# Performance work log

Measured on AMD Instinct MI355X. Metric: run time of the kernel, lower is better.

Reference implementation:

```python
import jax, jax.numpy as jnp
import numpy as np

EMBED_DIM = 1024
NUM_HEADS = 16
HEAD_DIM = EMBED_DIM // NUM_HEADS
ROPE_BASE = 10000.0


def setup_inputs() -> dict:
    key = jax.random.key(0)
    ks = jax.random.split(key, 12)
    B, T, M, D = 4, 2048, 2048, EMBED_DIM
    query = jax.random.normal(ks[0], (B, T, D), dtype=jnp.float32)
    k_in = jax.random.normal(ks[1], (B, M, D), dtype=jnp.float32)
    v_in = jax.random.normal(ks[2], (B, M, D), dtype=jnp.float32)
    query_position_ids = jnp.sort(
        jax.random.randint(ks[3], (B, T), 0, 4096), axis=-1
    ).astype(jnp.int64)
    # xavier-uniform-ish projection weights, zero biases (as in _reset_parameters)
    lim = float(np.sqrt(6.0 / (D + D)))
    Wq = jax.random.uniform(ks[4], (D, D), minval=-lim, maxval=lim, dtype=jnp.float32)
    Wk = jax.random.uniform(ks[5], (D, D), minval=-lim, maxval=lim, dtype=jnp.float32)
    Wv = jax.random.uniform(ks[6], (D, D), minval=-lim, maxval=lim, dtype=jnp.float32)
    Wo = jax.random.uniform(ks[7], (D, D), minval=-lim, maxval=lim, dtype=jnp.float32)
    bq = jnp.zeros((D,), jnp.float32)
    bk = jnp.zeros((D,), jnp.float32)
    bv = jnp.zeros((D,), jnp.float32)
    bo = jnp.zeros((D,), jnp.float32)
    return dict(query=query, key=k_in, value=v_in,
                query_position_ids=query_position_ids,
                Wq=Wq, bq=bq, Wk=Wk, bk=bk, Wv=Wv, bv=bv, Wo=Wo, bo=bo)


def _apply_rope(q, position_ids):
    # q: [B, T, H, hd]; position_ids: [B, T]
    hd = q.shape[-1]
    inv_freq = 1.0 / (ROPE_BASE ** (jnp.arange(0, hd, 2, dtype=jnp.float32) / hd))
    ang = position_ids.astype(jnp.float32)[:, :, None] * inv_freq  # [B, T, hd/2]
    cos = jnp.cos(ang)[:, :, None, :]  # [B, T, 1, hd/2]
    sin = jnp.sin(ang)[:, :, None, :]
    q1, q2 = q[..., : hd // 2], q[..., hd // 2:]
    return jnp.concatenate([q1 * cos - q2 * sin, q2 * cos + q1 * sin], axis=-1)


def reference(query, key, value, query_position_ids, Wq, bq, Wk, bk, Wv, bv, Wo, bo):
    B, T, D = query.shape
    M = key.shape[1]
    H, hd = NUM_HEADS, HEAD_DIM
    scaling = 1.0 / np.sqrt(hd)
    q = (query @ Wq.T + bq).reshape(B, T, H, hd)
    k = (key @ Wk.T + bk).reshape(B, M, H, hd)
    v = (value @ Wv.T + bv).reshape(B, M, H, hd)
    q = _apply_rope(q, query_position_ids)
    # scores: [B, H, T, M]
    scores = jnp.einsum('bthd,bmhd->bhtm', q, k) * scaling
    attn = jax.nn.softmax(scores, axis=-1)
    out = jnp.einsum('bhtm,bmhd->bthd', attn, v).reshape(B, T, D)
    return out @ Wo.T + bo
```

## Files before the change

### kernel.cpp

```cpp
#include <hip/hip_runtime.h>
#include <hip/hip_bf16.h>
#include <math.h>

typedef __hip_bfloat16 bf16;
typedef __attribute__((ext_vector_type(8))) short bf16x8;
typedef __attribute__((ext_vector_type(4))) float f32x4;

#define D_MODEL 1024
#define N_HEADS 16
#define HEAD_D  64
#define SEQ     2048
#define BATCH   4
#define NROWS   (BATCH*SEQ)

#define SCALE_Q 0.18033688011112042f

#define MFMA(a,b,c) __builtin_amdgcn_mfma_f32_16x16x32_bf16(a,b,c,0,0,0)

#if __has_builtin(__builtin_amdgcn_exp2f)
#define EXP2(x) __builtin_amdgcn_exp2f(x)
#else
#define EXP2(x) exp2f(x)
#endif

__device__ __forceinline__ void gload16(void* lds_uniform_base, const void* g) {
  __builtin_amdgcn_global_load_lds(
      (const __attribute__((address_space(1))) void*)g,
      (__attribute__((address_space(3))) void*)lds_uniform_base,
      16, 0, 0);
}

__device__ __forceinline__ unsigned pkrne(float a, float b) {
  unsigned ua = __float_as_uint(a), ub = __float_as_uint(b);
  ua += 0x7FFFu + ((ua >> 16) & 1u);
  ub += 0x7FFFu + ((ub >> 16) & 1u);
  return (ua >> 16) | (ub & 0xFFFF0000u);
}
__device__ __forceinline__ unsigned cvtpk(float a, float b) {
  unsigned r;
  asm("v_cvt_pk_bf16_f32 %0, %1, %2" : "=v"(r) : "v"(a), "v"(b));
  return r;
}
__device__ __forceinline__ bf16x8 cvt8rne(float4 a, float4 b) {
  union { bf16x8 v; unsigned u[4]; } u;
  u.u[0] = pkrne(a.x, a.y); u.u[1] = pkrne(a.z, a.w);
  u.u[2] = pkrne(b.x, b.y); u.u[3] = pkrne(b.z, b.w);
  return u.v;
}

__global__ __launch_bounds__(256)
void convw(const float* __restrict__ src, bf16* __restrict__ dst) {
  int idx = (blockIdx.x * 256 + threadIdx.x) * 8;
  float4 a = *(const float4*)(src + idx);
  float4 b = *(const float4*)(src + idx + 4);
  *(bf16x8*)(dst + idx) = cvt8rne(a, b);
}

__global__ __launch_bounds__(256)
void convw3(const float* __restrict__ s0, const float* __restrict__ s1,
            const float* __restrict__ s2, bf16* __restrict__ dst) {
  int g = blockIdx.x;
  const float* src = (g < 512) ? s0 : ((g < 1024) ? s1 : s2);
  int idx = ((g & 511) * 256 + threadIdx.x) * 8;
  float4 a = *(const float4*)(src + idx);
  float4 b = *(const float4*)(src + idx + 4);
  *(bf16x8*)(dst + (size_t)(g >> 9) * 1048576 + idx) = cvt8rne(a, b);
}

template<int MODE>
__global__ __launch_bounds__(256, 2)
void gemm_bt(const bf16* __restrict__ Xb, const bf16* __restrict__ Wb,
             const float* __restrict__ bias, void* __restrict__ outv,
             const int* __restrict__ pos) {
  __shared__ bf16 sA[128*64];
  __shared__ bf16 sB[128*64];

  const int tid  = threadIdx.x;
  const int lane = tid & 63, wid = tid >> 6;
  const int q4 = lane >> 4, l15 = lane & 15;
  const int rb = blockIdx.x * 128;
  const int cb = blockIdx.y * 128;
  const int wm = (wid >> 1) * 64, wn = (wid & 1) * 64;

  f32x4 acc[4][4];
  const f32x4 z4 = {0.f, 0.f, 0.f, 0.f};
#pragma unroll
  for (int i = 0; i < 4; ++i)
#pragma unroll
    for (int j = 0; j < 4; ++j) acc[i][j] = z4;

  for (int kt = 0; kt < 16; ++kt) {
    const int k0 = kt * 64;
#pragma unroll
    for (int i = 0; i < 4; ++i) {
      int o  = i*4096 + tid*16;
      int rr = o >> 7;
      int c0 = ((o >> 4) & 7) ^ (rr & 7);
      gload16((char*)sA + i*4096 + (wid << 10),
              Xb + (size_t)(rb + rr)*D_MODEL + k0 + c0*8);
      gload16((char*)sB + i*4096 + (wid << 10),
              Wb + (size_t)(cb + rr)*D_MODEL + k0 + c0*8);
    }
    __syncthreads();
#pragma unroll
    for (int kq = 0; kq < 2; ++kq) {
      bf16x8 af[4], bfr[4];
      const int cc = (kq*4 + q4) ^ (l15 & 7);
#pragma unroll
      for (int mi = 0; mi < 4; ++mi) {
        int r = wm + mi*16 + l15;
        af[mi] = *(const bf16x8*)((const char*)sA + r*128 + cc*16);
      }
#pragma unroll
      for (int ni = 0; ni < 4; ++ni) {
        int r = wn + ni*16 + l15;
        bfr[ni] = *(const bf16x8*)((const char*)sB + r*128 + cc*16);
      }
#pragma unroll
      for (int mi = 0; mi < 4; ++mi)
#pragma unroll
        for (int ni = 0; ni < 4; ++ni)
          acc[mi][ni] = MFMA(af[mi], bfr[ni], acc[mi][ni]);
    }
    __syncthreads();
  }

  if (MODE == 0) {
    float* outF = (float*)outv;
#pragma unroll
    for (int ni = 0; ni < 4; ++ni) {
      int col = cb + wn + ni*16 + l15;
      float bv = bias[col];
#pragma unroll
      for (int mi = 0; mi < 4; ++mi) {
        int row0 = rb + wm + mi*16 + q4*4;
#pragma unroll
        for (int r = 0; r < 4; ++r)
          outF[(size_t)(row0 + r)*D_MODEL + col] = acc[mi][ni][r] + bv;
      }
    }
  } else if (MODE == 1) {
    bf16* out = (bf16*)outv;
#pragma unroll
    for (int ni = 0; ni < 4; ++ni) {
      int col = cb + wn + ni*16 + l15;
      int h = col >> 6, d = col & 63;
      float bv = bias[col];
#pragma unroll
      for (int mi = 0; mi < 4; ++mi) {
#pragma unroll
        for (int r = 0; r < 4; ++r) {
          int row = rb + wm + mi*16 + q4*4 + r;
          int b = row >> 11, m = row & 2047;
          out[(size_t)((b*N_HEADS + h)*SEQ + m)*HEAD_D + d] =
              __float2bfloat16(acc[mi][ni][r] + bv);
        }
      }
    }
  } else if (MODE == 2) {
    bf16* out = (bf16*)outv;
#pragma unroll
    for (int mi = 0; mi < 4; ++mi) {
#pragma unroll
      for (int r = 0; r < 4; ++r) {
        int row = rb + wm + mi*16 + q4*4 + r;
        float bv = bias[row];
#pragma unroll
        for (int ni = 0; ni < 4; ++ni) {
          int col = cb + wn + ni*16 + l15;
          int b = col >> 11, m = col & 2047;
          out[(size_t)(b*D_MODEL + row)*SEQ + m] =
              __float2bfloat16(acc[mi][ni][r] + bv);
        }
      }
    }
  } else {
    bf16* out = (bf16*)outv;
    const bool is64 = (pos[NROWS - 1] == 0);
    const float CLOG = 13.287712379549449f / 32.0f;
    float invf0 = exp2f(-(float)(l15)      * CLOG);
    float invf1 = exp2f(-(float)(l15 + 16) * CLOG);
    int h = (cb + wn) >> 6;
#pragma unroll
    for (int ni = 0; ni < 2; ++ni) {
      int col1 = cb + wn + ni*16 + l15;
      int d = ni*16 + l15;
      float invf = (ni == 0) ? invf0 : invf1;
      float b1 = bias[col1];
      float b2 = bias[col1 + 32];
#pragma unroll
      for (int mi = 0; mi < 4; ++mi) {
#pragma unroll
        for (int r = 0; r < 4; ++r) {
          int row = rb + wm + mi*16 + q4*4 + r;
          int b = row >> 11, t = row & 2047;
          int pv = is64 ? pos[2*row] : pos[row];
          float ang = (float)pv * invf;
          float sn, cs;
          __sincosf(ang, &sn, &cs);
          float q1 = acc[mi][ni][r]   + b1;
          float q2 = acc[mi][ni+2][r] + b2;
          size_t base = (size_t)((b*N_HEADS + h)*SEQ + t)*HEAD_D;
          out[base + d]      = __float2bfloat16((q1*cs - q2*sn) * SCALE_Q);
          out[base + d + 32] = __float2bfloat16((q2*cs + q1*sn) * SCALE_Q);
        }
      }
    }
  }
}

__global__ __launch_bounds__(256, 2)
void attn_kernel(const bf16* __restrict__ Q, const bf16* __restrict__ K,
                 const bf16* __restrict__ VT, bf16* __restrict__ O) {
  __shared__ __align__(16) char smem[49152];
  char* sK  = smem;
  char* sVT = smem + 16384;

  const int tid  = threadIdx.x;
  const int lane = tid & 63, wid = tid >> 6;
  const int q4 = lane >> 4, l15 = lane & 15;
  const int n   = blockIdx.x;
  const int bh  = (n & 7) + 8 * (n >> 7);
  const int qb  = ((n >> 3) & 15) * 128;

  const bf16* Qp  = Q  + (size_t)bh * SEQ * HEAD_D;
  const bf16* Kp  = K  + (size_t)bh * SEQ * HEAD_D;
  const bf16* VTp = VT + (size_t)bh * HEAD_D * SEQ;
  char* wP = smem + (wid & 1) * 8192 + (wid >> 1) * 32768;

  bf16x8 qf[2][2];
#pragma unroll
  for (int mi = 0; mi < 2; ++mi)
#pragma unroll
    for (int kq = 0; kq < 2; ++kq) {
      int t = qb + wid*32 + mi*16 + l15;
      qf[mi][kq] = *(const bf16x8*)(Qp + (size_t)t*HEAD_D + kq*32 + q4*8);
    }

  const f32x4 z4 = {0.f, 0.f, 0.f, 0.f};
  f32x4 oacc[2][4];
  float mrow[2], lrow[2];
#pragma unroll
  for (int mi = 0; mi < 2; ++mi) {
#pragma unroll
    for (int nd = 0; nd < 4; ++nd) oacc[mi][nd] = z4;
    mrow[mi] = -3.0e38f; lrow[mi] = 0.f;
  }

  for (int kv = 0; kv < 16; ++kv) {
    const int m0 = kv * 128;
#pragma unroll
    for (int i = 0; i < 4; ++i) {
      int o  = i*4096 + tid*16;
      int rr = o >> 7;
      int c0 = ((o >> 4) & 7) ^ (rr & 7);
      gload16(sK + i*4096 + (wid << 10),
              Kp + (size_t)(m0 + rr)*HEAD_D + c0*8);
    }
#pragma unroll
    for (int i = 0; i < 4; ++i) {
      int o  = i*4096 + tid*16;
      int rr = o >> 8;
      int c0 = ((o >> 4) & 15) ^ (rr & 7);
      gload16(sVT + i*4096 + (wid << 10),
              VTp + (size_t)rr*SEQ + m0 + c0*8);
    }
    __syncthreads();

    f32x4 st[2][8];
#pragma unroll
    for (int mi = 0; mi < 2; ++mi)
#pragma unroll
      for (int ni = 0; ni < 8; ++ni) st[mi][ni] = z4;
#pragma unroll
    for (int kq = 0; kq < 2; ++kq) {
      const int cc = (kq*4 + q4) ^ (l15 & 7);
#pragma unroll
      for (int ni = 0; ni < 8; ++ni) {
        bf16x8 kf = *(const bf16x8*)(sK + (ni*16 + l15)*128 + cc*16);
        st[0][ni] = MFMA(kf, qf[0][kq], st[0][ni]);
        st[1][ni] = MFMA(kf, qf[1][kq], st[1][ni]);
      }
    }
    __syncthreads();

#pragma unroll
    for (int mi = 0; mi < 2; ++mi) {
      float mloc = st[mi][0][0];
#pragma unroll
      for (int ni = 0; ni < 8; ++ni)
#pragma unroll
        for (int r = 0; r < 4; ++r) mloc = fmaxf(mloc, st[mi][ni][r]);
      mloc = fmaxf(mloc, __shfl_xor(mloc, 16, 64));
      mloc = fmaxf(mloc, __shfl_xor(mloc, 32, 64));
      float mn = fmaxf(mrow[mi], mloc);
      float al = EXP2(mrow[mi] - mn);
      mrow[mi] = mn;
      float rs = 0.f;
#pragma unroll
      for (int ni = 0; ni < 8; ++ni)
#pragma unroll
        for (int r = 0; r < 4; ++r) {
          float p = EXP2(st[mi][ni][r] - mn);
          st[mi][ni][r] = p;
          rs += p;
        }
      lrow[mi] = lrow[mi]*al + rs;
#pragma unroll
      for (int nd = 0; nd < 4; ++nd)
#pragma unroll
        for (int r = 0; r < 4; ++r) oacc[mi][nd][r] *= al;
      char* rowp = wP + (mi*16 + l15)*256;
#pragma unroll
      for (int ni = 0; ni < 8; ++ni) {
        uint2 pk;
        pk.x = cvtpk(st[mi][ni][0], st[mi][ni][1]);
        pk.y = cvtpk(st[mi][ni][2], st[mi][ni][3]);
        int c  = 2*ni + (q4 >> 1);
        int cs = c ^ (l15 & 7);
        *(uint2*)(rowp + cs*16 + 8*(q4 & 1)) = pk;
      }
    }

#pragma unroll
    for (int kk = 0; kk < 4; ++kk) {
      const int cc = (kk*4 + q4) ^ (l15 & 7);
      bf16x8 vf[4];
#pragma unroll
      for (int nd = 0; nd < 4; ++nd)
        vf[nd] = *(const bf16x8*)(sVT + (nd*16 + l15)*256 + cc*16);
#pragma unroll
      for (int mi = 0; mi < 2; ++mi) {
        bf16x8 pb = *(const bf16x8*)(wP + (mi*16 + l15)*256 + cc*16);
#pragma unroll
        for (int nd = 0; nd < 4; ++nd)
          oacc[mi][nd] = MFMA(vf[nd], pb, oacc[mi][nd]);
      }
    }
    __syncthreads();
  }

  const int b = bh >> 4, h = bh & 15;
#pragma unroll
  for (int mi = 0; mi < 2; ++mi) {
    float l = lrow[mi];
    l += __shfl_xor(l, 16, 64);
    l += __shfl_xor(l, 32, 64);
    float inv = 1.0f / l;
    int t = qb + wid*32 + mi*16 + l15;
#pragma unroll
    for (int nd = 0; nd < 4; ++nd) {
      uint2 pk;
      pk.x = pkrne(oacc[mi][nd][0]*inv, oacc[mi][nd][1]*inv);
      pk.y = pkrne(oacc[mi][nd][2]*inv, oacc[mi][nd][3]*inv);
      int d = nd*16 + 4*q4;
      *(uint2*)(O + (size_t)(b*SEQ + t)*D_MODEL + h*HEAD_D + d) = pk;
    }
  }
}

extern "C" void kernel_launch(void* const* d_in, const int* in_sizes, int n_in,
                              void* d_out, int out_size, void* d_ws, size_t ws_size,
                              hipStream_t stream) {
  const float* query = (const float*)d_in[0];
  const float* key   = (const float*)d_in[1];
  const float* value = (const float*)d_in[2];
  const int*   pos   = (const int*)d_in[3];
  const float* Wq = (const float*)d_in[4];  const float* bq = (const float*)d_in[5];
  const float* Wk = (const float*)d_in[6];  const float* bk = (const float*)d_in[7];
  const float* Wv = (const float*)d_in[8];  const float* bv = (const float*)d_in[9];
  const float* Wo = (const float*)d_in[10]; const float* bo = (const float*)d_in[11];

  char* ws = (char*)d_ws;
  bf16* qbuf  = (bf16*)(ws);
  bf16* kbuf  = (bf16*)(ws + (size_t)16777216);
  bf16* vtbuf = (bf16*)(ws + (size_t)33554432);
  bf16* obuf  = (bf16*)(ws + (size_t)50331648);
  bf16* wqb = obuf;
  bf16* wkb = obuf + (size_t)1048576;
  bf16* wvb = obuf + (size_t)2097152;
  bf16* wob = qbuf;
  bf16* xact = (bf16*)d_out;

  dim3 blk(256);
  dim3 gproj(NROWS/128, D_MODEL/128);
  dim3 gprojT(D_MODEL/128, NROWS/128);

  convw3<<<1536, blk, 0, stream>>>(Wq, Wk, Wv, wqb);

  convw<<<4096, blk, 0, stream>>>(value, xact);
  gemm_bt<2><<<gprojT, blk, 0, stream>>>(wvb, xact, bv, vtbuf, nullptr);

  convw<<<4096, blk, 0, stream>>>(key, xact);
  gemm_bt<1><<<gproj,  blk, 0, stream>>>(xact, wkb, bk, kbuf, nullptr);

  convw<<<4096, blk, 0, stream>>>(query, xact);
  gemm_bt<3><<<gproj,  blk, 0, stream>>>(xact, wqb, bq, qbuf, pos);

  attn_kernel<<<dim3(1024), blk, 0, stream>>>(qbuf, kbuf, vtbuf, obuf);

  convw<<<512, blk, 0, stream>>>(Wo, wob);
  gemm_bt<0><<<gproj,  blk, 0, stream>>>(obuf, wob, bo, d_out, nullptr);
  (void)in_sizes; (void)n_in; (void)out_size; (void)ws_size;
}
```

Before: 369.2 us.

## Prefetch next K/V tile into registers while computing current attention tile

Replaces the direct global-to-LDS loads with register staging: the next K and V^T tile is loaded into registers at the start of each iteration and written to shared memory after the PV MFMAs, so global latency overlaps with compute. It also raises wave priority around the MFMA blocks and splits the softmax max and sum reductions into tree and multi-accumulator forms to shorten dependency chains. In exchange it uses more VGPRs for staging, which may lower occupancy, and adds an extra barrier per iteration.

```diff
diff --git a/kernel.cpp b/kernel.cpp
--- a/kernel.cpp
+++ b/kernel.cpp
@@ -247,31 +247,41 @@
     mrow[mi] = -3.0e38f; lrow[mi] = 0.f;
   }
 
-  for (int kv = 0; kv < 16; ++kv) {
-    const int m0 = kv * 128;
+  float4 kst[4], vst[4];
+  auto load_tile = [&](int kv2) {
+    const int m0n = kv2 * 128;
 #pragma unroll
     for (int i = 0; i < 4; ++i) {
       int o  = i*4096 + tid*16;
-      int rr = o >> 7;
-      int c0 = ((o >> 4) & 7) ^ (rr & 7);
-      gload16(sK + i*4096 + (wid << 10),
-              Kp + (size_t)(m0 + rr)*HEAD_D + c0*8);
-    }
+      int rK = o >> 7;
+      int cK = ((o >> 4) & 7) ^ (rK & 7);
+      kst[i] = *(const float4*)(Kp + (size_t)(m0n + rK)*HEAD_D + cK*8);
+      int rV = o >> 8;
+      int cV = ((o >> 4) & 15) ^ (rV & 7);
+      vst[i] = *(const float4*)(VTp + (size_t)rV*SEQ + m0n + cV*8);
+    }
+  };
+  auto store_tile = [&]() {
 #pragma unroll
     for (int i = 0; i < 4; ++i) {
-      int o  = i*4096 + tid*16;
-      int rr = o >> 8;
-      int c0 = ((o >> 4) & 15) ^ (rr & 7);
-      gload16(sVT + i*4096 + (wid << 10),
-              VTp + (size_t)rr*SEQ + m0 + c0*8);
-    }
-    __syncthreads();
+      *(float4*)(sK  + i*4096 + tid*16) = kst[i];
+      *(float4*)(sVT + i*4096 + tid*16) = vst[i];
+    }
+  };
+
+  load_tile(0);
+  store_tile();
+  __syncthreads();
+
+  for (int kv = 0; kv < 16; ++kv) {
+    if (kv < 15) load_tile(kv + 1);
 
     f32x4 st[2][8];
 #pragma unroll
     for (int mi = 0; mi < 2; ++mi)
 #pragma unroll
       for (int ni = 0; ni < 8; ++ni) st[mi][ni] = z4;
+    __builtin_amdgcn_s_setprio(1);
 #pragma unroll
     for (int kq = 0; kq < 2; ++kq) {
       const int cc = (kq*4 + q4) ^ (l15 & 7);
@@ -282,30 +292,36 @@
         st[1][ni] = MFMA(kf, qf[1][kq], st[1][ni]);
       }
     }
+    __builtin_amdgcn_s_setprio(0);
     __syncthreads();
 
 #pragma unroll
     for (int mi = 0; mi < 2; ++mi) {
-      float mloc = st[mi][0][0];
+      float tn[8];
 #pragma unroll
       for (int ni = 0; ni < 8; ++ni)
-#pragma unroll
-        for (int r = 0; r < 4; ++r) mloc = fmaxf(mloc, st[mi][ni][r]);
+        tn[ni] = fmaxf(fmaxf(st[mi][ni][0], st[mi][ni][1]),
+                       fmaxf(st[mi][ni][2], st[mi][ni][3]));
+      float t01 = fmaxf(tn[0], tn[1]), t23 = fmaxf(tn[2], tn[3]);
+      float t45 = fmaxf(tn[4], tn[5]), t67 = fmaxf(tn[6], tn[7]);
+      float mloc = fmaxf(fmaxf(t01, t23), fmaxf(t45, t67));
       mloc = fmaxf(mloc, __shfl_xor(mloc, 16, 64));
       mloc = fmaxf(mloc, __shfl_xor(mloc, 32, 64));
       float mn = fmaxf(mrow[mi], mloc);
       float al = EXP2(mrow[mi] - mn);
       mrow[mi] = mn;
-      float rs = 0.f;
-#pragma unroll
-      for (int ni = 0; ni < 8; ++ni)
-#pragma unroll
-        for (int r = 0; r < 4; ++r) {
-          float p = EXP2(st[mi][ni][r] - mn);
-          st[mi][ni][r] = p;
-          rs += p;
-        }
-      lrow[mi] = lrow[mi]*al + rs;
+      float rs0 = 0.f, rs1 = 0.f, rs2 = 0.f, rs3 = 0.f;
+#pragma unroll
+      for (int ni = 0; ni < 8; ++ni) {
+        float p0 = EXP2(st[mi][ni][0] - mn);
+        float p1 = EXP2(st[mi][ni][1] - mn);
+        float p2 = EXP2(st[mi][ni][2] - mn);
+        float p3 = EXP2(st[mi][ni][3] - mn);
+        st[mi][ni][0] = p0; st[mi][ni][1] = p1;
+        st[mi][ni][2] = p2; st[mi][ni][3] = p3;
+        rs0 += p0; rs1 += p1; rs2 += p2; rs3 += p3;
+      }
+      lrow[mi] = lrow[mi]*al + ((rs0 + rs1) + (rs2 + rs3));
 #pragma unroll
       for (int nd = 0; nd < 4; ++nd)
 #pragma unroll
@@ -322,6 +338,7 @@
       }
     }
 
+    __builtin_amdgcn_s_setprio(1);
 #pragma unroll
     for (int kk = 0; kk < 4; ++kk) {
       const int cc = (kk*4 + q4) ^ (l15 & 7);
@@ -337,7 +354,13 @@
           oacc[mi][nd] = MFMA(vf[nd], pb, oacc[mi][nd]);
       }
     }
+    __builtin_amdgcn_s_setprio(0);
     __syncthreads();
+
+    if (kv < 15) {
+      store_tile();
+      __syncthreads();
+    }
   }
 
   const int b = bh >> 4, h = bh & 15;
```

Result: slower. 439.4 us (+19.0%).

## Fuse fp32-to-bf16 activation conversion into projection GEMM tile loads

Applied to the files above, without the earlier changes.

Drops the three separate convw passes that turned the query, key and value activations into bf16 scratch buffers. The projection GEMMs now load fp32 tiles straight into LDS, which doubles the LDS footprint for that operand, and convert to bf16 with v_cvt_pk_bf16_f32 while building MFMA fragments. This removes a full write and read of each activation tensor plus three kernel launches. In exchange the GEMM reads twice the bytes per tile, uses more LDS (which may lower occupancy), and changes the rounding instruction used.

```diff
diff --git a/kernel.cpp b/kernel.cpp
--- a/kernel.cpp
+++ b/kernel.cpp
@@ -45,6 +45,12 @@
   union { bf16x8 v; unsigned u[4]; } u;
   u.u[0] = pkrne(a.x, a.y); u.u[1] = pkrne(a.z, a.w);
   u.u[2] = pkrne(b.x, b.y); u.u[3] = pkrne(b.z, b.w);
+  return u.v;
+}
+__device__ __forceinline__ bf16x8 cvt8pk(float4 a, float4 b) {
+  union { bf16x8 v; unsigned u[4]; } u;
+  u.u[0] = cvtpk(a.x, a.y); u.u[1] = cvtpk(a.z, a.w);
+  u.u[2] = cvtpk(b.x, b.y); u.u[3] = cvtpk(b.z, b.w);
   return u.v;
 }
 
@@ -67,13 +73,13 @@
   *(bf16x8*)(dst + (size_t)(g >> 9) * 1048576 + idx) = cvt8rne(a, b);
 }
 
-template<int MODE>
+template<int MODE, int AF32, int BF32>
 __global__ __launch_bounds__(256, 2)
-void gemm_bt(const bf16* __restrict__ Xb, const bf16* __restrict__ Wb,
+void gemm_bt(const void* __restrict__ Xv, const void* __restrict__ Wv_,
              const float* __restrict__ bias, void* __restrict__ outv,
              const int* __restrict__ pos) {
-  __shared__ bf16 sA[128*64];
-  __shared__ bf16 sB[128*64];
+  __shared__ __align__(16) char sA[AF32 ? 32768 : 16384];
+  __shared__ __align__(16) char sB[BF32 ? 32768 : 16384];
 
   const int tid  = threadIdx.x;
   const int lane = tid & 63, wid = tid >> 6;
@@ -91,30 +97,73 @@
 
   for (int kt = 0; kt < 16; ++kt) {
     const int k0 = kt * 64;
-#pragma unroll
-    for (int i = 0; i < 4; ++i) {
-      int o  = i*4096 + tid*16;
-      int rr = o >> 7;
-      int c0 = ((o >> 4) & 7) ^ (rr & 7);
-      gload16((char*)sA + i*4096 + (wid << 10),
-              Xb + (size_t)(rb + rr)*D_MODEL + k0 + c0*8);
-      gload16((char*)sB + i*4096 + (wid << 10),
-              Wb + (size_t)(cb + rr)*D_MODEL + k0 + c0*8);
+    if (AF32) {
+#pragma unroll
+      for (int i = 0; i < 8; ++i) {
+        int o  = i*4096 + tid*16;
+        int rr = o >> 8;
+        int c0 = ((o >> 4) & 15) ^ (rr & 7);
+        gload16(sA + i*4096 + (wid << 10),
+                (const float*)Xv + (size_t)(rb + rr)*D_MODEL + k0 + c0*4);
+      }
+    } else {
+#pragma unroll
+      for (int i = 0; i < 4; ++i) {
+        int o  = i*4096 + tid*16;
+        int rr = o >> 7;
+        int c0 = ((o >> 4) & 7) ^ (rr & 7);
+        gload16(sA + i*4096 + (wid << 10),
+                (const bf16*)Xv + (size_t)(rb + rr)*D_MODEL + k0 + c0*8);
+      }
+    }
+    if (BF32) {
+#pragma unroll
+      for (int i = 0; i < 8; ++i) {
+        int o  = i*4096 + tid*16;
+        int rr = o >> 8;
+        int c0 = ((o >> 4) & 15) ^ (rr & 7);
+        gload16(sB + i*4096 + (wid << 10),
+                (const float*)Wv_ + (size_t)(cb + rr)*D_MODEL + k0 + c0*4);
+      }
+    } else {
+#pragma unroll
+      for (int i = 0; i < 4; ++i) {
+        int o  = i*4096 + tid*16;
+        int rr = o >> 7;
+        int c0 = ((o >> 4) & 7) ^ (rr & 7);
+        gload16(sB + i*4096 + (wid << 10),
+                (const bf16*)Wv_ + (size_t)(cb + rr)*D_MODEL + k0 + c0*8);
+      }
     }
     __syncthreads();
 #pragma unroll
     for (int kq = 0; kq < 2; ++kq) {
       bf16x8 af[4], bfr[4];
-      const int cc = (kq*4 + q4) ^ (l15 & 7);
+      const int cc  = (kq*4 + q4) ^ (l15 & 7);
+      const int cf0 = kq*8 + q4*2;
 #pragma unroll
       for (int mi = 0; mi < 4; ++mi) {
         int r = wm + mi*16 + l15;
-        af[mi] = *(const bf16x8*)((const char*)sA + r*128 + cc*16);
+        if (AF32) {
+          const char* rp = sA + r*256;
+          float4 a0 = *(const float4*)(rp + ((cf0    ) ^ (l15 & 7))*16);
+          float4 a1 = *(const float4*)(rp + ((cf0 + 1) ^ (l15 & 7))*16);
+          af[mi] = cvt8pk(a0, a1);
+        } else {
+          af[mi] = *(const bf16x8*)(sA + r*128 + cc*16);
+        }
       }
 #pragma unroll
       for (int ni = 0; ni < 4; ++ni) {
         int r = wn + ni*16 + l15;
-        bfr[ni] = *(const bf16x8*)((const char*)sB + r*128 + cc*16);
+        if (BF32) {
+          const char* rp = sB + r*256;
+          float4 b0 = *(const float4*)(rp + ((cf0    ) ^ (l15 & 7))*16);
+          float4 b1 = *(const float4*)(rp + ((cf0 + 1) ^ (l15 & 7))*16);
+          bfr[ni] = cvt8pk(b0, b1);
+        } else {
+          bfr[ni] = *(const bf16x8*)(sB + r*128 + cc*16);
+        }
       }
 #pragma unroll
       for (int mi = 0; mi < 4; ++mi)
@@ -380,7 +429,6 @@
   bf16* wkb = obuf + (size_t)1048576;
   bf16* wvb = obuf + (size_t)2097152;
   bf16* wob = qbuf;
-  bf16* xact = (bf16*)d_out;
 
   dim3 blk(256);
   dim3 gproj(NROWS/128, D_MODEL/128);
@@ -388,18 +436,15 @@
 
   convw3<<<1536, blk, 0, stream>>>(Wq, Wk, Wv, wqb);
 
-  convw<<<4096, blk, 0, stream>>>(value, xact);
-  gemm_bt<2><<<gprojT, blk, 0, stream>>>(wvb, xact, bv, vtbuf, nullptr);
-
-  convw<<<4096, blk, 0, stream>>>(key, xact);
-  gemm_bt<1><<<gproj,  blk, 0, stream>>>(xact, wkb, bk, kbuf, nullptr);
-
-  convw<<<4096, blk, 0, stream>>>(query, xact);
-  gemm_bt<3><<<gproj,  blk, 0, stream>>>(xact, wqb, bq, qbuf, pos);
+  gemm_bt<2,0,1><<<gprojT, blk, 0, stream>>>(wvb, value, bv, vtbuf, nullptr);
+
+  gemm_bt<1,1,0><<<gproj,  blk, 0, stream>>>(key, wkb, bk, kbuf, nullptr);
+
+  gemm_bt<3,1,0><<<gproj,  blk, 0, stream>>>(query, wqb, bq, qbuf, pos);
 
   attn_kernel<<<dim3(1024), blk, 0, stream>>>(qbuf, kbuf, vtbuf, obuf);
 
   convw<<<512, blk, 0, stream>>>(Wo, wob);
-  gemm_bt<0><<<gproj,  blk, 0, stream>>>(obuf, wob, bo, d_out, nullptr);
+  gemm_bt<0,0,0><<<gproj,  blk, 0, stream>>>(obuf, wob, bo, d_out, nullptr);
   (void)in_sizes; (void)n_in; (void)out_size; (void)ws_size;
 }
```

Result: slower. 382.2 us (+3.5%).
